# Kernel optimization log

Hardware: AMD Instinct MI355X
Metric: run time of the kernel (lower is better)

Reference implementation:

```python
import jax, jax.numpy as jnp
import numpy as np

NUM_CLASSES = 80
N_CAND = 10  # simOTA n_candidate_k


def setup_inputs() -> dict:
    key = jax.random.key(0)
    ks = jax.random.split(key, 8)
    G, C, B = 300, NUM_CLASSES, 2
    # FPN grids for a 1280x1280 input, strides 8/16/32 -> 160^2+80^2+40^2 = 33600 anchors
    levels = [(160, 8), (80, 16), (40, 32)]
    xs, ys, ss = [], [], []
    for n, s in levels:
        yy, xx = np.meshgrid(np.arange(n), np.arange(n), indexing='ij')
        xs.append(xx.ravel()); ys.append(yy.ravel()); ss.append(np.full(n * n, s))
    x_shifts = jnp.asarray(np.concatenate(xs), jnp.float32)[None]
    y_shifts = jnp.asarray(np.concatenate(ys), jnp.float32)[None]
    strides = jnp.asarray(np.concatenate(ss), jnp.float32)
    expanded_strides = strides[None]
    A = x_shifts.shape[1]
    # gt boxes in cxcywh, image coords
    gt_cxy = jax.random.uniform(ks[0], (G, 2), jnp.float32, 0.0, 1280.0)
    gt_wh = jax.random.uniform(ks[1], (G, 2), jnp.float32, 16.0, 256.0)
    gt_bboxes_per_image = jnp.concatenate([gt_cxy, gt_wh], -1)
    gt_classes = jax.random.randint(ks[2], (G,), 0, C)
    # predicted boxes: anchor centers + noise, wh ~ a few strides
    anc_x = (x_shifts[0] + 0.5) * strides
    anc_y = (y_shifts[0] + 0.5) * strides
    pr_cxy = jnp.stack([anc_x, anc_y], -1) + jax.random.normal(ks[3], (A, 2), jnp.float32) * strides[:, None]
    pr_wh = strides[:, None] * (1.0 + 4.0 * jax.random.uniform(ks[4], (A, 2), jnp.float32))
    bboxes_preds_per_image = jnp.concatenate([pr_cxy, pr_wh], -1)
    cls_preds = jax.random.normal(ks[5], (B, A, C), jnp.float32)
    obj_preds = jax.random.normal(ks[6], (B, A, 1), jnp.float32)
    return {
        'batch_idx': 0, 'num_gt': G, 'total_num_anchors': A,
        'gt_bboxes_per_image': gt_bboxes_per_image, 'gt_classes': gt_classes,
        'bboxes_preds_per_image': bboxes_preds_per_image,
        'expanded_strides': expanded_strides, 'x_shifts': x_shifts, 'y_shifts': y_shifts,
        'cls_preds': cls_preds, 'obj_preds': obj_preds,
    }


def _pairwise_iou(gt, pr):
    # gt [G,4], pr [A,4], cxcywh -> iou [G,A] (bboxes_iou with xyxy=False)
    tl = jnp.maximum(gt[:, None, :2] - 0.5 * gt[:, None, 2:], pr[None, :, :2] - 0.5 * pr[None, :, 2:])
    br = jnp.minimum(gt[:, None, :2] + 0.5 * gt[:, None, 2:], pr[None, :, :2] + 0.5 * pr[None, :, 2:])
    wh = jnp.clip(br - tl, 0.0)
    inter = wh[..., 0] * wh[..., 1]
    area_g = gt[:, 2] * gt[:, 3]
    area_p = pr[:, 2] * pr[:, 3]
    return inter / (area_g[:, None] + area_p[None, :] - inter)


def reference(batch_idx, num_gt, total_num_anchors, gt_bboxes_per_image, gt_classes,
              bboxes_preds_per_image, expanded_strides, x_shifts, y_shifts, cls_preds, obj_preds):
    G, A = gt_bboxes_per_image.shape[0], bboxes_preds_per_image.shape[0]
    strides = expanded_strides[0]
    xc = (x_shifts[0] + 0.5) * strides  # [A] anchor centers
    yc = (y_shifts[0] + 0.5) * strides
    gx, gy, gw, gh = (gt_bboxes_per_image[:, i] for i in range(4))
    # is_in_boxes [G,A]
    in_box = ((xc[None] > (gx - 0.5 * gw)[:, None]) & ((gx + 0.5 * gw)[:, None] > xc[None]) &
              (yc[None] > (gy - 0.5 * gh)[:, None]) & ((gy + 0.5 * gh)[:, None] > yc[None]))
    r = 2.5 * strides[None]  # center_radius * stride
    in_ctr = ((xc[None] > gx[:, None] - r) & (gx[:, None] + r > xc[None]) &
              (yc[None] > gy[:, None] - r) & (gy[:, None] + r > yc[None]))
    fg_any = in_box.any(0) | in_ctr.any(0)          # fg_mask over all anchors
    candidate = in_box & in_ctr                      # is_in_boxes_and_center (full-anchor layout)
    ious = jnp.where(fg_any[None, :], _pairwise_iou(gt_bboxes_per_image, bboxes_preds_per_image), 0.0)
    # pairwise cls BCE cost; one-hot target -> factored form, never materializes [G,A,C]
    p = jnp.sqrt(jax.nn.sigmoid(cls_preds[batch_idx]) * jax.nn.sigmoid(obj_preds[batch_idx]))  # [A,C]
    p = jnp.clip(p, 1e-7, 1.0 - 1e-7)
    lp, l1p = jnp.log(p), jnp.log1p(-p)
    s_all = l1p.sum(-1)                              # [A] sum_c log(1-p_c)
    cls_loss = -((lp - l1p)[:, gt_classes].T + s_all[None, :])  # [G,A]
    # cost; 1e5 penalty for non-candidates (as in source), extra 1e6 keeps non-fg anchors
    # strictly below any fg anchor in top-k order (source only ever considers fg anchors)
    cost = cls_loss - 3.0 * jnp.log(ious + 1e-8) + 100000.0 * (~candidate) + 1000000.0 * (~fg_any)[None, :]
    # dynamic-k: sum of top-10 ious per gt, clamped to >= 1 (<= 10 inherently)
    topk_ious, _ = jax.lax.top_k(ious, N_CAND)
    dks = jnp.clip(topk_ious.sum(1).astype(jnp.int32), 1, N_CAND)  # [G]
    _, idx = jax.lax.top_k(-cost, N_CAND)            # [G,10] lowest-cost anchors per gt
    sel = (jnp.arange(N_CAND)[None, :] < dks[:, None]).astype(jnp.int32)
    matching = jnp.zeros((G, A), jnp.int32).at[jnp.arange(G)[:, None], idx].max(sel)
    # resolve anchors matched to >1 gt: keep argmax of T_scores over gts (as in source)
    multi = matching.sum(0) > 1
    best_gt = jnp.argmax(cost, axis=0)               # [A]
    matching = jnp.where(multi[None, :], (jnp.arange(G)[:, None] == best_gt[None, :]).astype(jnp.int32), matching)
    fg_final = matching.sum(0) > 0                   # final fg mask over all anchors
    num_fg = fg_final.sum()
    matched = jnp.argmax(matching, axis=0)           # [A]
    gt_matched_classes = jnp.where(fg_final, gt_classes[matched], -1)
    pred_ious = (matching.astype(ious.dtype) * ious).sum(0)  # [A], 0 where unmatched
    matched_gt_inds = jnp.where(fg_final, matched, -1)
    # fixed-shape (full-anchor) versions of the source's compacted outputs
    return (gt_matched_classes, fg_final, pred_ious, matched_gt_inds, num_fg)
```

## Files before the change

### kernel.cpp

```cpp
#include <hip/hip_runtime.h>
#include <math.h>

#define NUMC 80
#define NCAND 10
#define NK 16
#define GT_LDS 300
#define MAXGRP 544

typedef unsigned long long u64;

__device__ __forceinline__ float sigmoid_stable(float x) {
    float e = expf(-fabsf(x));
    float num = (x >= 0.0f) ? 1.0f : e;
    return num / (1.0f + e);
}

__device__ __forceinline__ float s_all_for(int a, int b, int A, float so,
                                           const float* __restrict__ cls)
{
    const float4* cp4 = (const float4*)(cls + ((size_t)b * A + a) * NUMC);
    float acc = 0.0f;
    for (int q = 0; q < NUMC/4; ++q) {
        float4 v4 = cp4[q];
        float vv[4] = {v4.x, v4.y, v4.z, v4.w};
        #pragma unroll
        for (int k = 0; k < 4; ++k) {
            float sc = sigmoid_stable(vv[k]);
            float p = sqrtf(sc * so);
            p = fminf(fmaxf(p, 1e-7f), 1.0f - 1e-7f);
            acc += log1pf(-p);
        }
    }
    return acc;
}

__device__ __forceinline__ void bitonic16_desc(float (&L)[NK]) {
    #pragma unroll
    for (int j = 0; j < NK; ++j) if (!(j & 8)) { float a=L[j], b=L[j|8]; L[j]=fmaxf(a,b); L[j|8]=fminf(a,b); }
    #pragma unroll
    for (int j = 0; j < NK; ++j) if (!(j & 4)) { float a=L[j], b=L[j|4]; L[j]=fmaxf(a,b); L[j|4]=fminf(a,b); }
    #pragma unroll
    for (int j = 0; j < NK; ++j) if (!(j & 2)) { float a=L[j], b=L[j|2]; L[j]=fmaxf(a,b); L[j|2]=fminf(a,b); }
    #pragma unroll
    for (int j = 0; j < NK; ++j) if (!(j & 1)) { float a=L[j], b=L[j|1]; L[j]=fmaxf(a,b); L[j|1]=fminf(a,b); }
}

__device__ __forceinline__ void merge16_desc(float (&A_)[NK], const float (&B_)[NK]) {
    float L[NK];
    #pragma unroll
    for (int j = 0; j < NK; ++j) L[j] = fmaxf(A_[j], B_[NK-1-j]);
    bitonic16_desc(L);
    #pragma unroll
    for (int j = 0; j < NK; ++j) A_[j] = L[j];
}

struct CostRes { float cost; float iou; bool cand; };

__device__ __forceinline__ CostRes cost_pair(
    int g, int a, int b, int A,
    const float* __restrict__ gt, float4 p4, float4 an, int fga,
    float sA, float so, const float* __restrict__ cls,
    const int* __restrict__ gcls)
{
    float gx = gt[g*4+0], gy = gt[g*4+1], gw = gt[g*4+2], gh = gt[g*4+3];
    float px = p4.x, py = p4.y, pw = p4.z, ph = p4.w;
    float tlx = fmaxf(gx - 0.5f*gw, px - 0.5f*pw);
    float tly = fmaxf(gy - 0.5f*gh, py - 0.5f*ph);
    float brx = fminf(gx + 0.5f*gw, px + 0.5f*pw);
    float bry = fminf(gy + 0.5f*gh, py + 0.5f*ph);
    float iw = fmaxf(brx - tlx, 0.0f);
    float ih = fmaxf(bry - tly, 0.0f);
    float inter = iw * ih;
    float iou = inter / (gw*gh + pw*ph - inter);
    float fi = fga ? iou : 0.0f;
    float x = an.x, y = an.y, r = an.z;
    bool inb = (x > gx - 0.5f*gw) && (gx + 0.5f*gw > x) &&
               (y > gy - 0.5f*gh) && (gy + 0.5f*gh > y);
    bool inc = (x > gx - r) && (gx + r > x) && (y > gy - r) && (gy + r > y);
    bool cand = inb && inc;
    float cv = cls[((size_t)b * A + a) * NUMC + gcls[g]];
    float sc = sigmoid_stable(cv);
    float p = sqrtf(sc * so);
    p = fminf(fmaxf(p, 1e-7f), 1.0f - 1e-7f);
    float lp = logf(p);
    float l1p = log1pf(-p);
    float clsl = -((lp - l1p) + sA);
    float cost = clsl - 3.0f * logf(fi + 1e-8f)
               + (cand ? 0.0f : 100000.0f)
               + (fga  ? 0.0f : 1000000.0f);
    CostRes res; res.cost = cost; res.iou = fi; res.cand = cand; return res;
}

__device__ __forceinline__ float pair_iou_masked4(
    int g, const float* __restrict__ gt, float4 p4, int fga)
{
    float gx = gt[g*4+0], gy = gt[g*4+1], gw = gt[g*4+2], gh = gt[g*4+3];
    float px = p4.x, py = p4.y, pw = p4.z, ph = p4.w;
    float tlx = fmaxf(gx - 0.5f*gw, px - 0.5f*pw);
    float tly = fmaxf(gy - 0.5f*gh, py - 0.5f*ph);
    float brx = fminf(gx + 0.5f*gw, px + 0.5f*pw);
    float bry = fminf(gy + 0.5f*gh, py + 0.5f*ph);
    float iw = fmaxf(brx - tlx, 0.0f);
    float ih = fmaxf(bry - tly, 0.0f);
    float inter = iw * ih;
    float iou = inter / (gw*gh + pw*ph - inter);
    return fga ? iou : 0.0f;
}

__global__ __launch_bounds__(512) void fused_pre_kernel(
    const int* __restrict__ bidx, int G, int A,
    const float* __restrict__ gt, const float* __restrict__ strides,
    const float* __restrict__ xs, const float* __restrict__ ys,
    const float* __restrict__ obj, const float* __restrict__ cls,
    const float4* __restrict__ pred4,
    float4* __restrict__ anc4, float* __restrict__ so_arr, float* __restrict__ s_arr,
    float4* __restrict__ ptlbr4, float* __restrict__ pare, float4* __restrict__ grpbox,
    int* __restrict__ fg_any, int* __restrict__ cand_any,
    int* __restrict__ count, int* __restrict__ mgt,
    int* __restrict__ fb_cnt, float* __restrict__ out)
{
    __shared__ float sgt[GT_LDS * 4];
    __shared__ float sx[64], sy[64], sr[64];
    __shared__ int   sflg[512];
    __shared__ float sl1p[64 * 81];

    int tid = threadIdx.x;
    int a0 = blockIdx.x * 64;
    int b = bidx[0];
    int GS = (G < GT_LDS) ? G : GT_LDS;

    for (int i = tid; i < GS * 4; i += 512) sgt[i] = gt[i];
    if (tid < 64) {
        int a = a0 + tid;
        float st = 0.0f, x = 0.0f, y = 0.0f;
        if (a < A) {
            st = strides[a];
            x = (xs[a] + 0.5f) * st;
            y = (ys[a] + 0.5f) * st;
            so_arr[a] = sigmoid_stable(obj[(size_t)b * A + a]);
        }
        sx[tid] = x; sy[tid] = y; sr[tid] = 2.5f * st;
    }
    __syncthreads();

    {
        int a_loc = tid & 63, chunk = tid >> 6;
        int a = a0 + a_loc;
        int any_or = 0, any_and = 0;
        if (a < A) {
            float x = sx[a_loc], y = sy[a_loc], r = sr[a_loc];
            int gpc = (G + 7) >> 3;
            int g0 = chunk * gpc;
            int g1 = min(G, g0 + gpc);
            for (int g = g0; g < g1; ++g) {
                float gx, gy, gw, gh;
                if (g < GS) { gx = sgt[g*4+0]; gy = sgt[g*4+1]; gw = sgt[g*4+2]; gh = sgt[g*4+3]; }
                else        { gx = gt[g*4+0];  gy = gt[g*4+1];  gw = gt[g*4+2];  gh = gt[g*4+3]; }
                bool inb = (x > gx - 0.5f*gw) && (gx + 0.5f*gw > x) &&
                           (y > gy - 0.5f*gh) && (gy + 0.5f*gh > y);
                bool inc = (x > gx - r) && (gx + r > x) && (y > gy - r) && (gy + r > y);
                any_or  |= (int)(inb | inc);
                any_and |= (int)(inb && inc);
            }
        }
        sflg[tid] = any_or | (any_and << 1);
    }
    __syncthreads();

    if (tid < 64) {
        int a = a0 + tid;
        float mnx = INFINITY, mny = INFINITY, mxx = -INFINITY, mxy = -INFINITY;
        int f = sflg[tid] | sflg[tid+64] | sflg[tid+128] | sflg[tid+192]
              | sflg[tid+256] | sflg[tid+320] | sflg[tid+384] | sflg[tid+448];
        int fg = f & 1, cd = (f >> 1) & 1;
        if (a < A) {
            fg_any[a] = fg;
            cand_any[a] = cd;
            anc4[a] = make_float4(sx[tid], sy[tid], sr[tid], 0.0f);
            s_arr[a] = 0.0f;
            count[a] = 0;
            mgt[a] = -1;
            float4 p4 = pred4[a];
            pare[a] = p4.z * p4.w;
            if (fg) {
                mnx = p4.x - 0.5f * p4.z;
                mny = p4.y - 0.5f * p4.w;
                mxx = p4.x + 0.5f * p4.z;
                mxy = p4.y + 0.5f * p4.w;
            }
            ptlbr4[a] = make_float4(mnx, mny, mxx, mxy);
        }
        #pragma unroll
        for (int off = 32; off > 0; off >>= 1) {
            mnx = fminf(mnx, __shfl_xor(mnx, off));
            mny = fminf(mny, __shfl_xor(mny, off));
            mxx = fmaxf(mxx, __shfl_xor(mxx, off));
            mxy = fmaxf(mxy, __shfl_xor(mxy, off));
        }
        if (tid == 0) grpbox[blockIdx.x] = make_float4(mnx, mny, mxx, mxy);
        sflg[tid] = cd;
    }
    __syncthreads();

    {
        int a_loc = tid >> 3, part = tid & 7;
        int a = a0 + a_loc;
        if (a < A && sflg[a_loc]) {
            float so = so_arr[a];
            const float* cp = cls + ((size_t)b * A + a) * NUMC + part * 10;
            #pragma unroll
            for (int j = 0; j < 10; ++j) {
                float sc = sigmoid_stable(cp[j]);
                float p = sqrtf(sc * so);
                p = fminf(fmaxf(p, 1e-7f), 1.0f - 1e-7f);
                sl1p[a_loc * 81 + part * 10 + j] = log1pf(-p);
            }
        }
    }
    __syncthreads();
    if (tid < 64) {
        int a = a0 + tid;
        if (a < A && sflg[tid]) {
            float acc = 0.0f;
            #pragma unroll 8
            for (int c = 0; c < NUMC; ++c) acc += sl1p[tid * 81 + c];
            s_arr[a] = acc;
        }
    }
    if (blockIdx.x == 0 && tid == 0) { out[(size_t)4 * A] = 0.0f; fb_cnt[0] = 0; }
}

__global__ __launch_bounds__(512) void scanIC_kernel(
    const int* __restrict__ bidx, int G, int A, int nGrp,
    const float* __restrict__ gt, const int* __restrict__ gcls,
    const float4* __restrict__ pred4, const float4* __restrict__ anc4,
    const float* __restrict__ s_arr, const float* __restrict__ so_arr,
    const float* __restrict__ cls, const int* __restrict__ fg_any,
    const float4* __restrict__ ptlbr4, const float* __restrict__ pare,
    const float4* __restrict__ grpbox,
    int* __restrict__ dk_arr, int* __restrict__ fb_list, int* __restrict__ fb_cnt,
    int* __restrict__ count, int* __restrict__ mgt)
{
    __shared__ float4 sgb[MAXGRP];
    __shared__ float  sI[8 * NCAND];
    __shared__ u64    scand[128];
    __shared__ int    smisc[2];

    int g = blockIdx.x;
    int tid = threadIdx.x;
    int b = bidx[0];

    for (int i = tid; i < nGrp; i += 512) sgb[i] = grpbox[i];
    if (tid == 0) smisc[0] = 0;
    __syncthreads();

    float gx = gt[g*4+0], gy = gt[g*4+1], gw = gt[g*4+2], gh = gt[g*4+3];
    float gtlx = gx - 0.5f*gw, gtly = gy - 0.5f*gh;
    float gbrx = gx + 0.5f*gw, gbry = gy + 0.5f*gh;
    float ag = gw * gh;

    float ti[NK];
    #pragma unroll
    for (int j = 0; j < NK; ++j) ti[j] = 0.0f;

    for (int a = tid; a < A; a += 512) {
        int grp = a >> 6;
        float4 gb = sgb[grp];
        if ((gb.z <= gtlx) || (gb.x >= gbrx) || (gb.w <= gtly) || (gb.y >= gbry))
            continue;
        float4 p = ptlbr4[a];
        float ap = pare[a];
        float tlx = fmaxf(gtlx, p.x);
        float tly = fmaxf(gtly, p.y);
        float brx = fminf(gbrx, p.z);
        float bry = fminf(gbry, p.w);
        float iw = fmaxf(brx - tlx, 0.0f);
        float ih = fmaxf(bry - tly, 0.0f);
        float inter = iw * ih;
        float fi = inter / (ag + ap - inter);
        if (fi > ti[NK-1]) {
            ti[NK-1] = fi;
            #pragma unroll
            for (int j = NK-1; j >= 1; --j) {
                if (ti[j] > ti[j-1]) { float t = ti[j]; ti[j] = ti[j-1]; ti[j-1] = t; }
            }
        }
    }

    #pragma unroll
    for (int lv = 0; lv < 6; ++lv) {
        int off = 1 << lv;
        float pv[NK];
        #pragma unroll
        for (int j = 0; j < NK; ++j) pv[j] = __shfl_xor(ti[j], off);
        merge16_desc(ti, pv);
    }
    int wid = tid >> 6, lane = tid & 63;
    if (lane == 0) {
        #pragma unroll
        for (int j = 0; j < NCAND; ++j) sI[wid * NCAND + j] = ti[j];
    }
    __syncthreads();

    if (tid < 64) {
        float acc[NK];
        const float* ib = sI + (tid < 8 ? tid : 0) * NCAND;
        #pragma unroll
        for (int j = 0; j < NK; ++j)
            acc[j] = (j < NCAND && tid < 8) ? ib[j] : 0.0f;
        #pragma unroll
        for (int lv = 0; lv < 3; ++lv) {
            int off = 1 << lv;
            float pv[NK];
            #pragma unroll
            for (int j = 0; j < NK; ++j) pv[j] = __shfl_xor(acc[j], off);
            merge16_desc(acc, pv);
        }
        if (tid == 0) {
            float s = 0.0f;
            #pragma unroll
            for (int j = 0; j < NCAND; ++j) s += acc[j];
            int dk = (int)s;
            if (dk < 1) dk = 1;
            if (dk > NCAND) dk = NCAND;
            smisc[1] = dk;
            dk_arr[g] = dk;
        }
    }
    __syncthreads();

    if (tid < 243) {
        int lvl = tid / 81, slot = tid % 81, sxi = slot % 9, syi = slot / 9;
        int n, si, base;
        if (lvl == 0)      { n = 160; si = 8;  base = 0; }
        else if (lvl == 1) { n = 80;  si = 16; base = 25600; }
        else               { n = 40;  si = 32; base = 32000; }
        float sf = (float)si;
        float mx = fminf(0.5f*gw, 2.5f*sf);
        float my = fminf(0.5f*gh, 2.5f*sf);
        int ilo = (int)floorf((gx - mx)/sf - 0.5f) - 1;
        int ihi = (int)ceilf ((gx + mx)/sf - 0.5f) + 1;
        int jlo = (int)floorf((gy - my)/sf - 0.5f) - 1;
        int jhi = (int)ceilf ((gy + my)/sf - 0.5f) + 1;
        if (ilo < 0) ilo = 0;
        if (jlo < 0) jlo = 0;
        if (ihi > n-1) ihi = n-1;
        if (jhi > n-1) jhi = n-1;
        int i = ilo + sxi, j = jlo + syi;
        if (i <= ihi && j <= jhi) {
            int a = base + j * n + i;
            CostRes cr = cost_pair(g, a, b, A, gt, pred4[a], anc4[a], fg_any[a],
                                   s_arr[a], so_arr[a], cls, gcls);
            if (cr.cand) {
                int k = atomicAdd(&smisc[0], 1);
                if (k < 128)
                    scand[k] = ((u64)__float_as_uint(cr.cost) << 32) | (unsigned)a;
            }
        }
    }
    __syncthreads();

    if (tid == 0) {
        int nc = smisc[0]; if (nc > 128) nc = 128;
        int dk = smisc[1];
        if (dk > nc) {
            int idx = atomicAdd(fb_cnt, 1);
            fb_list[idx] = g;
        } else {
            u64 top[NCAND];
            #pragma unroll
            for (int j = 0; j < NCAND; ++j) top[j] = ~0ULL;
            for (int t = 0; t < nc; ++t) {
                u64 v = scand[t];
                if (v < top[NCAND-1]) {
                    top[NCAND-1] = v;
                    #pragma unroll
                    for (int j = NCAND-1; j >= 1; --j) {
                        if (top[j] < top[j-1]) { u64 t2 = top[j]; top[j] = top[j-1]; top[j-1] = t2; }
                    }
                }
            }
            #pragma unroll
            for (int o = 0; o < NCAND; ++o) {
                if (o < dk) {
                    int a = (int)(top[o] & 0xffffffffULL);
                    atomicAdd(&count[a], 1);
                    atomicMax(&mgt[a], g);
                }
            }
        }
    }
}

__global__ __launch_bounds__(256) void fb_kernel(
    const int* __restrict__ bidx, int G, int A,
    const float* __restrict__ gt, const int* __restrict__ gcls,
    const float4* __restrict__ pred4, const float4* __restrict__ anc4,
    const float* __restrict__ s_arr, const float* __restrict__ so_arr,
    const float* __restrict__ cls, const int* __restrict__ fg_any,
    const int* __restrict__ cand_any,
    const int* __restrict__ dk_arr, const int* __restrict__ fb_list,
    const int* __restrict__ fb_cnt,
    int* __restrict__ count, int* __restrict__ mgt)
{
    int nfb = fb_cnt[0];
    if (nfb == 0) return;
    __shared__ u64 s_cv[256 * NCAND];
    int tid = threadIdx.x;
    int b = bidx[0];
    for (int f = blockIdx.x; f < nfb; f += gridDim.x) {
        int g = fb_list[f];
        int dk = dk_arr[g];
        u64 tc[NCAND];
        #pragma unroll
        for (int j = 0; j < NCAND; ++j) tc[j] = ~0ULL;
        for (int a = tid; a < A; a += 256) {
            float so = so_arr[a];
            float sA = cand_any[a] ? s_arr[a] : s_all_for(a, b, A, so, cls);
            CostRes cr = cost_pair(g, a, b, A, gt, pred4[a], anc4[a], fg_any[a],
                                   sA, so, cls, gcls);
            u64 v = ((u64)__float_as_uint(cr.cost) << 32) | (unsigned)a;
            if (v < tc[NCAND-1]) {
                tc[NCAND-1] = v;
                #pragma unroll
                for (int j = NCAND-1; j >= 1; --j) {
                    if (tc[j] < tc[j-1]) { u64 t2 = tc[j]; tc[j] = tc[j-1]; tc[j-1] = t2; }
                }
            }
        }
        #pragma unroll
        for (int j = 0; j < NCAND; ++j) s_cv[tid*NCAND+j] = tc[j];
        __syncthreads();
        for (int off = 128; off > 0; off >>= 1) {
            if (tid < off) {
                u64 rc[NCAND];
                int i = 0, k = 0;
                const u64* L = &s_cv[tid*NCAND];
                const u64* R = &s_cv[(tid+off)*NCAND];
                for (int o = 0; o < NCAND; ++o) {
                    if (L[i] < R[k]) { rc[o] = L[i]; ++i; }
                    else             { rc[o] = R[k]; ++k; }
                }
                for (int j = 0; j < NCAND; ++j) s_cv[tid*NCAND+j] = rc[j];
            }
            __syncthreads();
        }
        if (tid == 0) {
            for (int o = 0; o < dk; ++o) {
                int a = (int)(s_cv[o] & 0xffffffffULL);
                atomicAdd(&count[a], 1);
                atomicMax(&mgt[a], g);
            }
        }
        __syncthreads();
    }
}

__global__ __launch_bounds__(256) void finalize_kernel(
    const int* __restrict__ bidx, int G, int A,
    const float* __restrict__ gt, const int* __restrict__ gcls,
    const float4* __restrict__ pred4, const float4* __restrict__ anc4,
    const float* __restrict__ s_arr, const float* __restrict__ so_arr,
    const float* __restrict__ cls, const int* __restrict__ fg_any,
    const int* __restrict__ cand_any,
    const int* __restrict__ count, const int* __restrict__ mgt,
    float* __restrict__ out)
{
    __shared__ int mlist[256];
    __shared__ int mcnt;
    int tid = threadIdx.x;
    int b = bidx[0];
    if (tid == 0) mcnt = 0;
    __syncthreads();

    int a = blockIdx.x * 256 + tid;
    int cnt = (a < A) ? count[a] : 0;
    unsigned long long m = __ballot(cnt > 0);
    if ((tid & 63) == 0 && m) {
        atomicAdd(&out[(size_t)4*A], (float)__popcll(m));
    }
    if (a < A) {
        if (cnt > 1) {
            int k = atomicAdd(&mcnt, 1);
            mlist[k] = a;
            out[(size_t)A + a] = 1.0f;
        } else {
            float gmc = -1.0f, mgi = -1.0f, piou = 0.0f, fg = 0.0f;
            if (cnt == 1) {
                int matched = mgt[a];
                fg = 1.0f;
                gmc = (float)gcls[matched];
                mgi = (float)matched;
                piou = pair_iou_masked4(matched, gt, pred4[a], fg_any[a]);
            }
            out[a]               = gmc;
            out[(size_t)A + a]   = fg;
            out[(size_t)2*A + a] = piou;
            out[(size_t)3*A + a] = mgi;
        }
    }
    __syncthreads();

    int nm = mcnt;
    int wid = tid >> 6, lane = tid & 63;
    for (int i = wid; i < nm; i += 4) {
        int aa = mlist[i];
        float4 p4 = pred4[aa];
        float4 an = anc4[aa];
        int fga = fg_any[aa];
        float so = so_arr[aa];
        float sA = cand_any[aa] ? s_arr[aa] : s_all_for(aa, b, A, so, cls);
        float best = -INFINITY; int bi = 0x7fffffff;
        for (int gg = lane; gg < G; gg += 64) {
            CostRes cr = cost_pair(gg, aa, b, A, gt, p4, an, fga, sA, so, cls, gcls);
            if (cr.cost > best) { best = cr.cost; bi = gg; }
        }
        #pragma unroll
        for (int off = 32; off > 0; off >>= 1) {
            float ob = __shfl_xor(best, off);
            int obi = __shfl_xor(bi, off);
            if (ob > best || (ob == best && obi < bi)) { best = ob; bi = obi; }
        }
        if (lane == 0) {
            out[aa]               = (float)gcls[bi];
            out[(size_t)2*A + aa] = pair_iou_masked4(bi, gt, p4, fga);
            out[(size_t)3*A + aa] = (float)bi;
        }
    }
}

extern "C" void kernel_launch(void* const* d_in, const int* in_sizes, int n_in,
                              void* d_out, int out_size, void* d_ws, size_t ws_size,
                              hipStream_t stream)
{
    const int*   bidx    = (const int*)d_in[0];
    const float* gt      = (const float*)d_in[3];
    const int*   gcls    = (const int*)d_in[4];
    const float* pred    = (const float*)d_in[5];
    const float* strides = (const float*)d_in[6];
    const float* xs      = (const float*)d_in[7];
    const float* ys      = (const float*)d_in[8];
    const float* cls     = (const float*)d_in[9];
    const float* obj     = (const float*)d_in[10];
    int G = in_sizes[4];
    int A = in_sizes[6];
    float* out = (float*)d_out;
    const float4* pred4 = (const float4*)pred;

    char* ws = (char*)d_ws;
    size_t off = 0;
    auto alloc = [&](size_t bytes) -> void* {
        void* p = ws + off;
        off += (bytes + 255) & ~(size_t)255;
        return p;
    };
    int nGrp = (A + 63) / 64;
    float4* anc4     = (float4*)alloc((size_t)A * sizeof(float4));
    float*  so_arr   = (float*) alloc((size_t)A * sizeof(float));
    float*  s_arr    = (float*) alloc((size_t)A * sizeof(float));
    float4* ptlbr4   = (float4*)alloc((size_t)A * sizeof(float4));
    float*  pare     = (float*) alloc((size_t)A * sizeof(float));
    float4* grpbox   = (float4*)alloc((size_t)nGrp * sizeof(float4));
    int*    fg_any   = (int*)   alloc((size_t)A * sizeof(int));
    int*    cand_any = (int*)   alloc((size_t)A * sizeof(int));
    int*    count    = (int*)   alloc((size_t)A * sizeof(int));
    int*    mgt      = (int*)   alloc((size_t)A * sizeof(int));
    int*    dk_arr   = (int*)   alloc((size_t)G * sizeof(int));
    int*    fb_list  = (int*)   alloc((size_t)G * sizeof(int));
    int*    fb_cnt   = (int*)   alloc(256);

    int blocksA256 = (A + 255) / 256;

    fused_pre_kernel<<<nGrp, 512, 0, stream>>>(
        bidx, G, A, gt, strides, xs, ys, obj, cls, pred4,
        anc4, so_arr, s_arr, ptlbr4, pare, grpbox,
        fg_any, cand_any, count, mgt, fb_cnt, out);
    scanIC_kernel<<<G, 512, 0, stream>>>(
        bidx, G, A, nGrp, gt, gcls, pred4, anc4, s_arr, so_arr, cls, fg_any,
        ptlbr4, pare, grpbox, dk_arr, fb_list, fb_cnt, count, mgt);
    fb_kernel<<<64, 256, 0, stream>>>(
        bidx, G, A, gt, gcls, pred4, anc4, s_arr, so_arr, cls, fg_any, cand_any,
        dk_arr, fb_list, fb_cnt, count, mgt);
    finalize_kernel<<<blocksA256, 256, 0, stream>>>(
        bidx, G, A, gt, gcls, pred4, anc4, s_arr, so_arr, cls, fg_any, cand_any,
        count, mgt, out);
}
```

Before: 168.1 us.

## Split per-gt IoU top-k scan into segmented blocks and fold fallback into cost kernel

The per-gt IoU scan, previously one 512-thread block per gt over all anchors, now runs as a 2D grid of 16 anchor segments per gt with 64-thread blocks. Each block writes a partial top-10 to a workspace, and a separate cost kernel merges the partials to get dynamic k. The fallback path for gts with too few candidates now runs inside the cost kernel instead of a separate kernel with a global list. The finalize kernel also does one atomic per block for num_fg instead of one per wave. The aim is better GPU occupancy for the scan and removal of a launch and its global atomics, at the cost of an extra kernel boundary, a partial-result round trip, and a large shared buffer in the cost kernel.

Result: no change. 168.8 us (+0.4%).

```diff
diff --git a/kernel.cpp b/kernel.cpp
--- a/kernel.cpp
+++ b/kernel.cpp
@@ -4,8 +4,8 @@
 #define NUMC 80
 #define NCAND 10
 #define NK 16
+#define SEGI 16
 #define GT_LDS 300
-#define MAXGRP 544
 
 typedef unsigned long long u64;
 
@@ -117,7 +117,7 @@
     float4* __restrict__ ptlbr4, float* __restrict__ pare, float4* __restrict__ grpbox,
     int* __restrict__ fg_any, int* __restrict__ cand_any,
     int* __restrict__ count, int* __restrict__ mgt,
-    int* __restrict__ fb_cnt, float* __restrict__ out)
+    float* __restrict__ out)
 {
     __shared__ float sgt[GT_LDS * 4];
     __shared__ float sx[64], sy[64], sr[64];
@@ -227,32 +227,21 @@
             s_arr[a] = acc;
         }
     }
-    if (blockIdx.x == 0 && tid == 0) { out[(size_t)4 * A] = 0.0f; fb_cnt[0] = 0; }
-}
-
-__global__ __launch_bounds__(512) void scanIC_kernel(
-    const int* __restrict__ bidx, int G, int A, int nGrp,
-    const float* __restrict__ gt, const int* __restrict__ gcls,
-    const float4* __restrict__ pred4, const float4* __restrict__ anc4,
-    const float* __restrict__ s_arr, const float* __restrict__ so_arr,
-    const float* __restrict__ cls, const int* __restrict__ fg_any,
+    if (blockIdx.x == 0 && tid == 0) out[(size_t)4 * A] = 0.0f;
+}
+
+__global__ __launch_bounds__(64) void scanI_kernel(
+    int G, int A, int seglen,
+    const float* __restrict__ gt,
     const float4* __restrict__ ptlbr4, const float* __restrict__ pare,
     const float4* __restrict__ grpbox,
-    int* __restrict__ dk_arr, int* __restrict__ fb_list, int* __restrict__ fb_cnt,
-    int* __restrict__ count, int* __restrict__ mgt)
-{
-    __shared__ float4 sgb[MAXGRP];
-    __shared__ float  sI[8 * NCAND];
-    __shared__ u64    scand[128];
-    __shared__ int    smisc[2];
-
-    int g = blockIdx.x;
+    float* __restrict__ piou_ws)
+{
+    int seg = blockIdx.x;
+    int g = blockIdx.y;
+    int a0 = seg * seglen;
+    int a1 = min(A, a0 + seglen);
     int tid = threadIdx.x;
-    int b = bidx[0];
-
-    for (int i = tid; i < nGrp; i += 512) sgb[i] = grpbox[i];
-    if (tid == 0) smisc[0] = 0;
-    __syncthreads();
 
     float gx = gt[g*4+0], gy = gt[g*4+1], gw = gt[g*4+2], gh = gt[g*4+3];
     float gtlx = gx - 0.5f*gw, gtly = gy - 0.5f*gh;
@@ -263,9 +252,9 @@
     #pragma unroll
     for (int j = 0; j < NK; ++j) ti[j] = 0.0f;
 
-    for (int a = tid; a < A; a += 512) {
-        int grp = a >> 6;
-        float4 gb = sgb[grp];
+    for (int a = a0 + tid; a < a1; a += 64) {
+        int grp = __builtin_amdgcn_readfirstlane(a >> 6);
+        float4 gb = grpbox[grp];
         if ((gb.z <= gtlx) || (gb.x >= gbrx) || (gb.w <= gtly) || (gb.y >= gbry))
             continue;
         float4 p = ptlbr4[a];
@@ -295,21 +284,41 @@
         for (int j = 0; j < NK; ++j) pv[j] = __shfl_xor(ti[j], off);
         merge16_desc(ti, pv);
     }
-    int wid = tid >> 6, lane = tid & 63;
-    if (lane == 0) {
-        #pragma unroll
-        for (int j = 0; j < NCAND; ++j) sI[wid * NCAND + j] = ti[j];
-    }
-    __syncthreads();
-
+    if (tid == 0) {
+        int base = (g * SEGI + seg) * NCAND;
+        #pragma unroll
+        for (int j = 0; j < NCAND; ++j) piou_ws[base + j] = ti[j];
+    }
+}
+
+__global__ __launch_bounds__(256) void scanC_kernel(
+    const int* __restrict__ bidx, int G, int A,
+    const float* __restrict__ gt, const int* __restrict__ gcls,
+    const float4* __restrict__ pred4, const float4* __restrict__ anc4,
+    const float* __restrict__ s_arr, const float* __restrict__ so_arr,
+    const float* __restrict__ cls, const int* __restrict__ fg_any,
+    const int* __restrict__ cand_any,
+    const float* __restrict__ piou_ws,
+    int* __restrict__ count, int* __restrict__ mgt)
+{
+    __shared__ u64 scand[128];
+    __shared__ int smisc[2];
+    __shared__ int s_dofb;
+    __shared__ u64 s_cv[256 * NCAND];
+
+    int g = blockIdx.x;
+    int tid = threadIdx.x;
+    int b = bidx[0];
+
+    if (tid == 0) smisc[0] = 0;
     if (tid < 64) {
         float acc[NK];
-        const float* ib = sI + (tid < 8 ? tid : 0) * NCAND;
+        const float* ib = piou_ws + ((size_t)g * SEGI + (tid < SEGI ? tid : 0)) * NCAND;
         #pragma unroll
         for (int j = 0; j < NK; ++j)
-            acc[j] = (j < NCAND && tid < 8) ? ib[j] : 0.0f;
-        #pragma unroll
-        for (int lv = 0; lv < 3; ++lv) {
+            acc[j] = (j < NCAND && tid < SEGI) ? ib[j] : 0.0f;
+        #pragma unroll
+        for (int lv = 0; lv < 4; ++lv) {
             int off = 1 << lv;
             float pv[NK];
             #pragma unroll
@@ -324,11 +333,11 @@
             if (dk < 1) dk = 1;
             if (dk > NCAND) dk = NCAND;
             smisc[1] = dk;
-            dk_arr[g] = dk;
-        }
-    }
-    __syncthreads();
-
+        }
+    }
+    __syncthreads();
+
+    float gx = gt[g*4+0], gy = gt[g*4+1], gw = gt[g*4+2], gh = gt[g*4+3];
     if (tid < 243) {
         int lvl = tid / 81, slot = tid % 81, sxi = slot % 9, syi = slot / 9;
         int n, si, base;
@@ -364,9 +373,9 @@
         int nc = smisc[0]; if (nc > 128) nc = 128;
         int dk = smisc[1];
         if (dk > nc) {
-            int idx = atomicAdd(fb_cnt, 1);
-            fb_list[idx] = g;
+            s_dofb = 1;
         } else {
+            s_dofb = 0;
             u64 top[NCAND];
             #pragma unroll
             for (int j = 0; j < NCAND; ++j) top[j] = ~0ULL;
@@ -390,27 +399,10 @@
             }
         }
     }
-}
-
-__global__ __launch_bounds__(256) void fb_kernel(
-    const int* __restrict__ bidx, int G, int A,
-    const float* __restrict__ gt, const int* __restrict__ gcls,
-    const float4* __restrict__ pred4, const float4* __restrict__ anc4,
-    const float* __restrict__ s_arr, const float* __restrict__ so_arr,
-    const float* __restrict__ cls, const int* __restrict__ fg_any,
-    const int* __restrict__ cand_any,
-    const int* __restrict__ dk_arr, const int* __restrict__ fb_list,
-    const int* __restrict__ fb_cnt,
-    int* __restrict__ count, int* __restrict__ mgt)
-{
-    int nfb = fb_cnt[0];
-    if (nfb == 0) return;
-    __shared__ u64 s_cv[256 * NCAND];
-    int tid = threadIdx.x;
-    int b = bidx[0];
-    for (int f = blockIdx.x; f < nfb; f += gridDim.x) {
-        int g = fb_list[f];
-        int dk = dk_arr[g];
+    __syncthreads();
+
+    if (s_dofb) {
+        int dk = smisc[1];
         u64 tc[NCAND];
         #pragma unroll
         for (int j = 0; j < NCAND; ++j) tc[j] = ~0ULL;
@@ -452,7 +444,6 @@
                 atomicMax(&mgt[a], g);
             }
         }
-        __syncthreads();
     }
 }
 
@@ -468,6 +459,7 @@
 {
     __shared__ int mlist[256];
     __shared__ int mcnt;
+    __shared__ int wsum[4];
     int tid = threadIdx.x;
     int b = bidx[0];
     if (tid == 0) mcnt = 0;
@@ -476,9 +468,7 @@
     int a = blockIdx.x * 256 + tid;
     int cnt = (a < A) ? count[a] : 0;
     unsigned long long m = __ballot(cnt > 0);
-    if ((tid & 63) == 0 && m) {
-        atomicAdd(&out[(size_t)4*A], (float)__popcll(m));
-    }
+    if ((tid & 63) == 0) wsum[tid >> 6] = __popcll(m);
     if (a < A) {
         if (cnt > 1) {
             int k = atomicAdd(&mcnt, 1);
@@ -500,6 +490,10 @@
         }
     }
     __syncthreads();
+    if (tid == 0) {
+        int s = wsum[0] + wsum[1] + wsum[2] + wsum[3];
+        if (s) atomicAdd(&out[(size_t)4*A], (float)s);
+    }
 
     int nm = mcnt;
     int wid = tid >> 6, lane = tid & 63;
@@ -565,22 +559,20 @@
     int*    cand_any = (int*)   alloc((size_t)A * sizeof(int));
     int*    count    = (int*)   alloc((size_t)A * sizeof(int));
     int*    mgt      = (int*)   alloc((size_t)A * sizeof(int));
-    int*    dk_arr   = (int*)   alloc((size_t)G * sizeof(int));
-    int*    fb_list  = (int*)   alloc((size_t)G * sizeof(int));
-    int*    fb_cnt   = (int*)   alloc(256);
-
+    float*  piou_ws  = (float*) alloc((size_t)G * SEGI * NCAND * sizeof(float));
+
+    int seglenI = ((A + SEGI*64 - 1) / (SEGI*64)) * 64;
     int blocksA256 = (A + 255) / 256;
 
     fused_pre_kernel<<<nGrp, 512, 0, stream>>>(
         bidx, G, A, gt, strides, xs, ys, obj, cls, pred4,
         anc4, so_arr, s_arr, ptlbr4, pare, grpbox,
-        fg_any, cand_any, count, mgt, fb_cnt, out);
-    scanIC_kernel<<<G, 512, 0, stream>>>(
-        bidx, G, A, nGrp, gt, gcls, pred4, anc4, s_arr, so_arr, cls, fg_any,
-        ptlbr4, pare, grpbox, dk_arr, fb_list, fb_cnt, count, mgt);
-    fb_kernel<<<64, 256, 0, stream>>>(
+        fg_any, cand_any, count, mgt, out);
+    scanI_kernel<<<dim3(SEGI, G), 64, 0, stream>>>(
+        G, A, seglenI, gt, ptlbr4, pare, grpbox, piou_ws);
+    scanC_kernel<<<G, 256, 0, stream>>>(
         bidx, G, A, gt, gcls, pred4, anc4, s_arr, so_arr, cls, fg_any, cand_any,
-        dk_arr, fb_list, fb_cnt, count, mgt);
+        piou_ws, count, mgt);
     finalize_kernel<<<blocksA256, 256, 0, stream>>>(
         bidx, G, A, gt, gcls, pred4, anc4, s_arr, so_arr, cls, fg_any, cand_any,
         count, mgt, out);
```
